# Kernel tuning notes

Measured on AMD Instinct MI355X. Metric: run time of the kernel, lower is better.

Reference implementation:

```python
import jax, jax.numpy as jnp
import numpy as np

HIDDEN = 1024
HEADS = 16
HEAD_DIM = HIDDEN // HEADS


def setup_inputs() -> dict:
    key = jax.random.key(0)
    kx, kq, kk, kv, ko = jax.random.split(key, 5)
    s = 1.0 / np.sqrt(HIDDEN)
    return {
        "x": jax.random.normal(kx, (2, 2048, HIDDEN), dtype=jnp.float32),
        "Wq": jax.random.normal(kq, (HIDDEN, HIDDEN), dtype=jnp.float32) * s,
        "Wk": jax.random.normal(kk, (HIDDEN, HIDDEN), dtype=jnp.float32) * s,
        "Wv": jax.random.normal(kv, (HIDDEN, HIDDEN), dtype=jnp.float32) * s,
        "Wo": jax.random.normal(ko, (HIDDEN, HIDDEN), dtype=jnp.float32) * s,
    }


def reference(x, Wq, Wk, Wv, Wo):
    B, T, C = x.shape
    H, D = HEADS, HEAD_DIM
    # projections (torch Linear: y = x @ W.T); weights here stored as (out,in)==(C,C)
    q = (x @ Wq.T).reshape(B, T, H, D)
    k = (x @ Wk.T).reshape(B, T, H, D)
    v = (x @ Wv.T).reshape(B, T, H, D)
    scale = 1.0 / np.sqrt(D).astype(np.float32)
    # scores: (B,H,T,T)
    attn = jnp.einsum("bqhd,bkhd->bhqk", q, k) * scale
    causal = jnp.tril(jnp.ones((T, T), dtype=bool))  # keep lower triangle
    attn = jnp.where(causal, attn, -jnp.inf)
    attn = jax.nn.softmax(attn, axis=-1)
    out = jnp.einsum("bhqk,bkhd->bqhd", attn, v).reshape(B, T, C)
    return out @ Wo.T
```

## Files before the change

### kernel.cpp

```cpp
#include <hip/hip_runtime.h>
#include <cstdint>
#include <cstddef>

#define HID 1024
#define NH 16
#define HD 64
#define SEQ 2048
#define BATCH 2

typedef __attribute__((ext_vector_type(8))) short bf16x8;
typedef __attribute__((ext_vector_type(4))) short bf16x4;
typedef bf16x8 __attribute__((may_alias)) bf16x8_ma;
typedef bf16x4 __attribute__((may_alias)) bf16x4_ma;
typedef uint4 __attribute__((may_alias)) uint4_ma;
typedef __attribute__((ext_vector_type(4))) float f32x4;

__device__ __forceinline__ unsigned short f2bf(float f){
  unsigned u = __builtin_bit_cast(unsigned, f);
  u += 0x7fffu + ((u >> 16) & 1u);
  return (unsigned short)(u >> 16);
}

__device__ __forceinline__ unsigned cvtpk_bf16(float lo, float hi){
  unsigned r;
  asm("v_cvt_pk_bf16_f32 %0, %1, %2" : "=v"(r) : "v"(lo), "v"(hi));
  return r;
}

__device__ __forceinline__ void gll(const unsigned short* g, unsigned short* l){
  __builtin_amdgcn_global_load_lds(
      (const __attribute__((address_space(1))) unsigned int*)(g),
      (__attribute__((address_space(3))) unsigned int*)(l),
      16, 0, 0);
}


__global__ __launch_bounds__(256) void cvt_all(
    const float* __restrict__ x,  const float* __restrict__ wq,
    const float* __restrict__ wk, const float* __restrict__ wv,
    const float* __restrict__ wo,
    unsigned short* __restrict__ xb,  unsigned short* __restrict__ wqb,
    unsigned short* __restrict__ wkb, unsigned short* __restrict__ wvb,
    unsigned short* __restrict__ wob)
{
  const size_t NX = (size_t)BATCH*SEQ*HID;
  const size_t NW = (size_t)HID*HID;
  size_t i = ((size_t)blockIdx.x*256 + threadIdx.x)*4;
  const float* src; unsigned short* dst; size_t off;
  if (i < NX) { src = x; dst = xb; off = i; }
  else {
    size_t j = i - NX; int w = (int)(j >> 20); off = j & (NW-1);
    if      (w==0){ src=wq; dst=wqb; }
    else if (w==1){ src=wk; dst=wkb; }
    else if (w==2){ src=wv; dst=wvb; }
    else          { src=wo; dst=wob; }
  }
  float4 v = *(const float4*)(src+off);
  uint2 p;
  p.x = (unsigned)f2bf(v.x) | ((unsigned)f2bf(v.y)<<16);
  p.y = (unsigned)f2bf(v.z) | ((unsigned)f2bf(v.w)<<16);
  *(uint2*)(dst+off) = p;
}

__global__ __launch_bounds__(256) void gemm_qkv(
    const unsigned short* __restrict__ A,
    const unsigned short* __restrict__ Bq,
    const unsigned short* __restrict__ Bk,
    const unsigned short* __restrict__ Bv,
    unsigned short* __restrict__ Qh,
    unsigned short* __restrict__ Kh,
    unsigned short* __restrict__ VhT)
{
  __shared__ unsigned short S[16384];
  const int tid = threadIdx.x;
  const int w = tid >> 6, lane = tid & 63, l15 = lane & 15, quad = lane >> 4;
  const int wm = (w >> 1)*64, wn = (w & 1)*64;
  const int bm = blockIdx.y*128;
  const int which = blockIdx.x >> 3;
  const int bn = (blockIdx.x & 7)*128;
  const unsigned short* B = which==0 ? Bq : (which==1 ? Bk : Bv);
  unsigned short* C       = which==0 ? Qh : (which==1 ? Kh : VhT);
  const float cscale      = which==0 ? 0.18033688011112042f : 1.0f;
  const int lrow = lane >> 2;
  const int lcs = (((lane & 3) ^ ((lane >> 3) & 3))) * 8;
  const int qsw = (quad ^ ((l15 >> 1) & 3)) * 8;

  f32x4 acc[4][4] = {};

  {
    #pragma unroll
    for (int p=0;p<2;p++){
      int c = w*2 + p;
      gll(&A[(size_t)(bm + c*16 + lrow)*HID + lcs], &S[c*512]);
      gll(&B[(size_t)(bn + c*16 + lrow)*HID + lcs], &S[8192 + c*512]);
    }
  }
  __syncthreads();

  int cur = 0;
  for (int kb=0; kb<32; ++kb){
    if (kb < 31){
      unsigned short* Ad = S + (cur^1)*4096;
      unsigned short* Bd = S + 8192 + (cur^1)*4096;
      #pragma unroll
      for (int p=0;p<2;p++){
        int c = w*2 + p;
        gll(&A[(size_t)(bm + c*16 + lrow)*HID + (kb+1)*32 + lcs], &Ad[c*512]);
        gll(&B[(size_t)(bn + c*16 + lrow)*HID + (kb+1)*32 + lcs], &Bd[c*512]);
      }
    }
    const unsigned short* Ac = S + cur*4096;
    const unsigned short* Bc = S + 8192 + cur*4096;
    bf16x8 af[4], bfr[4];
    #pragma unroll
    for (int i=0;i<4;i++) af[i]  = *(const bf16x8*)(&Ac[(wm + i*16 + l15)*32 + qsw]);
    #pragma unroll
    for (int j=0;j<4;j++) bfr[j] = *(const bf16x8*)(&Bc[(wn + j*16 + l15)*32 + qsw]);
    #pragma unroll
    for (int i=0;i<4;i++)
      #pragma unroll
      for (int j=0;j<4;j++)
        acc[i][j] = __builtin_amdgcn_mfma_f32_16x16x32_bf16(af[i], bfr[j], acc[i][j], 0,0,0);
    __syncthreads();
    cur ^= 1;
  }

  #pragma unroll
  for (int i=0;i<4;i++)
    #pragma unroll
    for (int j=0;j<4;j++)
      #pragma unroll
      for (int r=0;r<4;r++){
        int row = wm + i*16 + quad*4 + r;
        int col = wn + j*16 + l15;
        unsigned off = (unsigned)(row*256 + col*2);
        *(unsigned short*)((char*)S + (off ^ ((unsigned)(row & 7) << 4))) =
            f2bf(acc[i][j][r]*cscale);
      }
  __syncthreads();
  if (which < 2){
    #pragma unroll
    for (int pass=0; pass<8; ++pass){
      int tr    = pass*16 + (tid >> 4);
      int hf    = (tid >> 3) & 1;
      int blkin = tid & 7;
      unsigned off = (unsigned)(tr*256 + hf*128 + blkin*16);
      uint4 v = *(const uint4_ma*)((const char*)S + (off ^ ((unsigned)(tr & 7) << 4)));
      int m = bm + tr, b = m >> 11, t = m & (SEQ-1);
      int h = (bn >> 6) + hf;
      *(uint4*)(&C[(((size_t)(b*NH + h))*SEQ + t)*HD + blkin*8]) = v;
    }
  } else {
    const int b = bm >> 11, tb = bm & (SEQ-1);
    #pragma unroll
    for (int pass=0; pass<8; ++pass){
      int idx  = pass*256 + tid;
      int dcol = idx & 127;
      int tc   = idx >> 7;
      unsigned short tmp[8];
      #pragma unroll
      for (int j=0;j<8;j++){
        int r = tc*8 + j;
        unsigned off = (unsigned)(r*256 + dcol*2) ^ ((unsigned)j << 4);
        tmp[j] = *(const unsigned short*)((const char*)S + off);
      }
      int hh = (bn >> 6) + (dcol >> 6);
      int d  = dcol & 63;
      *(uint4*)(&C[(((size_t)(b*NH + hh))*HD + d)*SEQ + tb + tc*8]) = *(uint4_ma*)tmp;
    }
  }
}

__global__ __launch_bounds__(256) void gemm_out(
    const unsigned short* __restrict__ A,
    const unsigned short* __restrict__ B,
    float* __restrict__ C)
{
  __shared__ unsigned short S[12288];
  const int tid = threadIdx.x;
  const int w = tid >> 6, lane = tid & 63, l15 = lane & 15, quad = lane >> 4;
  const int wm = (w >> 1)*64, wn = (w & 1)*32;
  const int bm = blockIdx.y*128, bn = blockIdx.x*64;
  const int lrow = lane >> 2;
  const int lcs = (((lane & 3) ^ ((lane >> 3) & 3))) * 8;
  const int qsw = (quad ^ ((l15 >> 1) & 3)) * 8;

  f32x4 acc[4][2] = {};

  {
    #pragma unroll
    for (int p=0;p<2;p++){
      int c = w*2 + p;
      gll(&A[(size_t)(bm + c*16 + lrow)*HID + lcs], &S[c*512]);
    }
    gll(&B[(size_t)(bn + w*16 + lrow)*HID + lcs], &S[8192 + w*512]);
  }
  __syncthreads();

  int cur = 0;
  for (int kb=0; kb<32; ++kb){
    if (kb < 31){
      unsigned short* Ad = S + (cur^1)*4096;
      unsigned short* Bd = S + 8192 + (cur^1)*2048;
      #pragma unroll
      for (int p=0;p<2;p++){
        int c = w*2 + p;
        gll(&A[(size_t)(bm + c*16 + lrow)*HID + (kb+1)*32 + lcs], &Ad[c*512]);
      }
      gll(&B[(size_t)(bn + w*16 + lrow)*HID + (kb+1)*32 + lcs], &Bd[w*512]);
    }
    const unsigned short* Ac = S + cur*4096;
    const unsigned short* Bc = S + 8192 + cur*2048;
    bf16x8 af[4], bfr[2];
    #pragma unroll
    for (int i=0;i<4;i++) af[i]  = *(const bf16x8*)(&Ac[(wm + i*16 + l15)*32 + qsw]);
    #pragma unroll
    for (int j=0;j<2;j++) bfr[j] = *(const bf16x8*)(&Bc[(wn + j*16 + l15)*32 + qsw]);
    #pragma unroll
    for (int i=0;i<4;i++)
      #pragma unroll
      for (int j=0;j<2;j++)
        acc[i][j] = __builtin_amdgcn_mfma_f32_16x16x32_bf16(af[i], bfr[j], acc[i][j], 0,0,0);
    __syncthreads();
    cur ^= 1;
  }

  #pragma unroll
  for (int i=0;i<4;i++)
    #pragma unroll
    for (int j=0;j<2;j++)
      #pragma unroll
      for (int r=0;r<4;r++){
        int m = bm + wm + i*16 + quad*4 + r;
        int n = bn + wn + j*16 + l15;
        C[(size_t)m*HID + n] = acc[i][j][r];
      }
}

__global__ __launch_bounds__(256, 4) void attn(
    const unsigned short* __restrict__ Qh,
    const unsigned short* __restrict__ Kh,
    const unsigned short* __restrict__ VhT,
    unsigned short* __restrict__ Ao)
{
  __shared__ unsigned short QP[4096];
  __shared__ unsigned short Ks[2][4096];
  __shared__ unsigned short Vt[2][4096];

  const int bh = blockIdx.x;
  const int y  = blockIdx.y;
  const int a = y & 7, bb = y >> 3;
  const int qb = (bb & 1) ? (7 - a)*4 + bb : a*4 + bb;
  const int tid = threadIdx.x;
  const int w = tid >> 6, lane = tid & 63, l15 = lane & 15, quad = lane >> 4;
  const int lrow = lane >> 2;
  const int lcs = (((lane & 3) ^ ((lane >> 3) & 3))) * 8;
  const int qsw = (quad ^ ((l15 >> 1) & 3)) * 8;

  const size_t base = (size_t)bh * SEQ * HD;
  const unsigned short* Qg  = Qh + base + (size_t)qb*64*HD;
  const unsigned short* VTg = VhT + base;
  unsigned short* Psw = QP + w*1024;
  const unsigned swz = (unsigned)(l15 & 7) << 4;

  #pragma unroll
  for (int p=0;p<2;p++){
    int c = w*2 + p;
    gll(&Qg[(size_t)((c&3)*16 + lrow)*HD + (c>>2)*32 + lcs], &QP[(c>>2)*2048 + (c&3)*512]);
  }
  {
    const unsigned short* Kg = Kh + base;
    if (w < 2){
      #pragma unroll
      for (int p=0;p<4;p++){ int cc = w*4 + p;
        gll(&Kg[(size_t)((cc&3)*16 + lrow)*HD + (cc>>2)*32 + lcs], &Ks[0][(cc>>2)*2048 + (cc&3)*512]); }
    } else {
      #pragma unroll
      for (int p=0;p<4;p++){ int cc = (w-2)*4 + p;
        gll(&VTg[(size_t)((cc&3)*16 + lrow)*SEQ + (cc>>2)*32 + lcs], &Vt[0][(cc>>2)*2048 + (cc&3)*512]); }
    }
  }
  __syncthreads();
  bf16x8 qfrag[2];
  #pragma unroll
  for (int kc=0;kc<2;kc++)
    qfrag[kc] = *(const bf16x8*)(&QP[kc*2048 + (w*16 + l15)*32 + qsw]);
  __syncthreads();

  f32x4 lacc = {0.f, 0.f, 0.f, 0.f};
  f32x4 oacc[4] = {};
  const int qrow = qb*64 + w*16 + l15;
  int cur = 0;

  for (int kb=0; kb<=qb; ++kb){
    if (kb < qb){
      const unsigned short* Kg2 = Kh + base + (size_t)(kb+1)*64*HD;
      unsigned short* Kd = Ks[cur^1];
      unsigned short* Vd = Vt[cur^1];
      if (w < 2){
        #pragma unroll
        for (int p=0;p<4;p++){ int cc = w*4 + p;
          gll(&Kg2[(size_t)((cc&3)*16 + lrow)*HD + (cc>>2)*32 + lcs], &Kd[(cc>>2)*2048 + (cc&3)*512]); }
      } else {
        #pragma unroll
        for (int p=0;p<4;p++){ int cc = (w-2)*4 + p;
          gll(&VTg[(size_t)((cc&3)*16 + lrow)*SEQ + (size_t)(kb+1)*64 + (cc>>2)*32 + lcs], &Vd[(cc>>2)*2048 + (cc&3)*512]); }
      }
    }

    const unsigned short* Ksc = Ks[cur];
    f32x4 s[4] = {};
    #pragma unroll
    for (int cb=0;cb<4;cb++)
      #pragma unroll
      for (int kc=0;kc<2;kc++){
        bf16x8 kfr = *(const bf16x8*)(&Ksc[kc*2048 + (cb*16 + l15)*32 + qsw]);
        s[cb] = __builtin_amdgcn_mfma_f32_16x16x32_bf16(kfr, qfrag[kc], s[cb], 0,0,0);
      }

    if (kb == qb){
      #pragma unroll
      for (int cb=0;cb<4;cb++)
        #pragma unroll
        for (int r=0;r<4;r++){
          int t = kb*64 + cb*16 + quad*4 + r;
          if (t > qrow) s[cb][r] = -1e30f;
        }
    }
    #pragma unroll
    for (int cb=0;cb<4;cb++)
      #pragma unroll
      for (int r=0;r<4;r++)
        s[cb][r] = exp2f(s[cb][r]);
    lacc += (s[0] + s[1]) + (s[2] + s[3]);

    #pragma unroll
    for (int cb=0;cb<4;cb++){
      uint2 d2;
      d2.x = cvtpk_bf16(s[cb][0], s[cb][1]);
      d2.y = cvtpk_bf16(s[cb][2], s[cb][3]);
      *(bf16x4_ma*)((char*)Psw + (((unsigned)(l15*128 + cb*32 + quad*8)) ^ swz)) =
          __builtin_bit_cast(bf16x4, d2);
    }
    asm volatile("" ::: "memory");
    bf16x8 pa[2];
    #pragma unroll
    for (int kc=0;kc<2;kc++)
      pa[kc] = *(const bf16x8_ma*)((const char*)Psw + (((unsigned)(l15*128 + kc*64 + quad*16)) ^ swz));

    const unsigned short* Vtc = Vt[cur];
    #pragma unroll
    for (int db=0;db<4;db++)
      #pragma unroll
      for (int kc=0;kc<2;kc++){
        bf16x8 vfr = *(const bf16x8*)(&Vtc[kc*2048 + (db*16 + l15)*32 + qsw]);
        oacc[db] = __builtin_amdgcn_mfma_f32_16x16x32_bf16(pa[kc], vfr, oacc[db], 0,0,0);
      }

    if (kb < qb) __syncthreads();
    cur ^= 1;
  }

  float l = (lacc[0] + lacc[1]) + (lacc[2] + lacc[3]);
  l += __shfl_xor(l, 16);
  l += __shfl_xor(l, 32);
  float inv[4];
  #pragma unroll
  for (int r=0;r<4;r++)
    inv[r] = 1.0f / __shfl(l, quad*4 + r);

  const int b = bh >> 4, h = bh & (NH-1);
  #pragma unroll
  for (int db=0;db<4;db++)
    #pragma unroll
    for (int r=0;r<4;r++){
      int t = qb*64 + w*16 + quad*4 + r;
      int col = h*HD + db*16 + l15;
      Ao[((size_t)b*SEQ + t)*HID + col] = f2bf(oacc[db][r] * inv[r]);
    }
}

extern "C" void kernel_launch(void* const* d_in, const int* in_sizes, int n_in,
                              void* d_out, int out_size, void* d_ws, size_t ws_size,
                              hipStream_t stream)
{
  const float* x  = (const float*)d_in[0];
  const float* Wq = (const float*)d_in[1];
  const float* Wk = (const float*)d_in[2];
  const float* Wv = (const float*)d_in[3];
  const float* Wo = (const float*)d_in[4];

  unsigned short* xb  = (unsigned short*)d_ws;
  unsigned short* wqb = xb  + (size_t)4*1024*1024;
  unsigned short* wkb = wqb + (size_t)1024*1024;
  unsigned short* wvb = wkb + (size_t)1024*1024;
  unsigned short* wob = wvb + (size_t)1024*1024;
  unsigned short* Qh  = wob + (size_t)1024*1024;
  unsigned short* Kh  = Qh  + (size_t)4*1024*1024;
  unsigned short* Vh  = Kh  + (size_t)4*1024*1024;
  unsigned short* VhT = Vh  + (size_t)4*1024*1024;
  unsigned short* Ao  = xb;

  cvt_all<<<8192, 256, 0, stream>>>(x, Wq, Wk, Wv, Wo, xb, wqb, wkb, wvb, wob);

  gemm_qkv<<<dim3(24, 32), 256, 0, stream>>>(xb, wqb, wkb, wvb, Qh, Kh, VhT);

  attn<<<dim3(BATCH*NH, SEQ/64), 256, 0, stream>>>(Qh, Kh, VhT, Ao);

  gemm_out<<<dim3(16, 32), 256, 0, stream>>>(Ao, wob, (float*)d_out);
}
```

Measured before the change: 175.2 us.

## Process 128-key tiles per pipeline stage in causal attention kernel

The attention kernel now loads K and V^T in 128-key tiles (two 64-key groups) per double-buffered stage instead of 64, halving the number of loop iterations and __syncthreads barriers. Each stage runs up to two 64-key sub-blocks, skipping the second when it lies past the causal limit. This doubles LDS use for K/V and lowers the launch-bounds occupancy hint from 4 to 2 blocks. Fewer waves can then hide latency, and the last tile may load keys it never uses.

New measurement: 185.2 us. +5.7%, slower.

```diff
diff --git a/kernel.cpp b/kernel.cpp
--- a/kernel.cpp
+++ b/kernel.cpp
@@ -237,15 +237,15 @@
       }
 }
 
-__global__ __launch_bounds__(256, 4) void attn(
+__global__ __launch_bounds__(256, 2) void attn(
     const unsigned short* __restrict__ Qh,
     const unsigned short* __restrict__ Kh,
     const unsigned short* __restrict__ VhT,
     unsigned short* __restrict__ Ao)
 {
   __shared__ unsigned short QP[4096];
-  __shared__ unsigned short Ks[2][4096];
-  __shared__ unsigned short Vt[2][4096];
+  __shared__ unsigned short Ks[2][8192];
+  __shared__ unsigned short Vt[2][8192];
 
   const int bh = blockIdx.x;
   const int y  = blockIdx.y;
@@ -259,6 +259,7 @@
 
   const size_t base = (size_t)bh * SEQ * HD;
   const unsigned short* Qg  = Qh + base + (size_t)qb*64*HD;
+  const unsigned short* Kg  = Kh + base;
   const unsigned short* VTg = VhT + base;
   unsigned short* Psw = QP + w*1024;
   const unsigned swz = (unsigned)(l15 & 7) << 4;
@@ -268,17 +269,14 @@
     int c = w*2 + p;
     gll(&Qg[(size_t)((c&3)*16 + lrow)*HD + (c>>2)*32 + lcs], &QP[(c>>2)*2048 + (c&3)*512]);
   }
-  {
-    const unsigned short* Kg = Kh + base;
-    if (w < 2){
-      #pragma unroll
-      for (int p=0;p<4;p++){ int cc = w*4 + p;
-        gll(&Kg[(size_t)((cc&3)*16 + lrow)*HD + (cc>>2)*32 + lcs], &Ks[0][(cc>>2)*2048 + (cc&3)*512]); }
-    } else {
-      #pragma unroll
-      for (int p=0;p<4;p++){ int cc = (w-2)*4 + p;
-        gll(&VTg[(size_t)((cc&3)*16 + lrow)*SEQ + (cc>>2)*32 + lcs], &Vt[0][(cc>>2)*2048 + (cc&3)*512]); }
-    }
+  if (w < 2){
+    #pragma unroll
+    for (int p=0;p<8;p++){ int cc = w*8 + p; int g = cc>>3, h = (cc>>2)&1, rb = cc&3;
+      gll(&Kg[(size_t)(g*64 + rb*16 + lrow)*HD + h*32 + lcs], &Ks[0][g*4096 + h*2048 + rb*512]); }
+  } else {
+    #pragma unroll
+    for (int p=0;p<8;p++){ int cc = (w-2)*8 + p; int g = cc>>3, h = (cc>>2)&1, rb = cc&3;
+      gll(&VTg[(size_t)(rb*16 + lrow)*SEQ + g*64 + h*32 + lcs], &Vt[0][g*4096 + h*2048 + rb*512]); }
   }
   __syncthreads();
   bf16x8 qfrag[2];
@@ -290,74 +288,82 @@
   f32x4 lacc = {0.f, 0.f, 0.f, 0.f};
   f32x4 oacc[4] = {};
   const int qrow = qb*64 + w*16 + l15;
+  const int qmax = qb*64 + 63;
+  const int nt = (qb >> 1) + 1;
   int cur = 0;
 
-  for (int kb=0; kb<=qb; ++kb){
-    if (kb < qb){
-      const unsigned short* Kg2 = Kh + base + (size_t)(kb+1)*64*HD;
-      unsigned short* Kd = Ks[cur^1];
-      unsigned short* Vd = Vt[cur^1];
+  for (int kb=0; kb<nt; ++kb){
+    if (kb+1 < nt){
       if (w < 2){
         #pragma unroll
-        for (int p=0;p<4;p++){ int cc = w*4 + p;
-          gll(&Kg2[(size_t)((cc&3)*16 + lrow)*HD + (cc>>2)*32 + lcs], &Kd[(cc>>2)*2048 + (cc&3)*512]); }
+        for (int p=0;p<8;p++){ int cc = w*8 + p; int g = cc>>3, h = (cc>>2)&1, rb = cc&3;
+          gll(&Kg[(size_t)((kb+1)*128 + g*64 + rb*16 + lrow)*HD + h*32 + lcs],
+              &Ks[cur^1][g*4096 + h*2048 + rb*512]); }
       } else {
         #pragma unroll
-        for (int p=0;p<4;p++){ int cc = (w-2)*4 + p;
-          gll(&VTg[(size_t)((cc&3)*16 + lrow)*SEQ + (size_t)(kb+1)*64 + (cc>>2)*32 + lcs], &Vd[(cc>>2)*2048 + (cc&3)*512]); }
-      }
-    }
-
+        for (int p=0;p<8;p++){ int cc = (w-2)*8 + p; int g = cc>>3, h = (cc>>2)&1, rb = cc&3;
+          gll(&VTg[(size_t)(rb*16 + lrow)*SEQ + (size_t)(kb+1)*128 + g*64 + h*32 + lcs],
+              &Vt[cur^1][g*4096 + h*2048 + rb*512]); }
+      }
+    }
     const unsigned short* Ksc = Ks[cur];
-    f32x4 s[4] = {};
-    #pragma unroll
-    for (int cb=0;cb<4;cb++)
-      #pragma unroll
-      for (int kc=0;kc<2;kc++){
-        bf16x8 kfr = *(const bf16x8*)(&Ksc[kc*2048 + (cb*16 + l15)*32 + qsw]);
-        s[cb] = __builtin_amdgcn_mfma_f32_16x16x32_bf16(kfr, qfrag[kc], s[cb], 0,0,0);
-      }
-
-    if (kb == qb){
-      #pragma unroll
-      for (int cb=0;cb<4;cb++)
-        #pragma unroll
-        for (int r=0;r<4;r++){
-          int t = kb*64 + cb*16 + quad*4 + r;
-          if (t > qrow) s[cb][r] = -1e30f;
+    const unsigned short* Vtc = Vt[cur];
+    const bool lastt = (kb == nt-1);
+
+    #pragma unroll
+    for (int g=0; g<2; ++g){
+      const int kstart = kb*128 + g*64;
+      if (kstart <= qmax){
+        f32x4 s[4] = {};
+        #pragma unroll
+        for (int cb=0;cb<4;cb++)
+          #pragma unroll
+          for (int kc=0;kc<2;kc++){
+            bf16x8 kfr = *(const bf16x8*)(&Ksc[g*4096 + kc*2048 + (cb*16 + l15)*32 + qsw]);
+            s[cb] = __builtin_amdgcn_mfma_f32_16x16x32_bf16(kfr, qfrag[kc], s[cb], 0,0,0);
+          }
+        if (lastt){
+          #pragma unroll
+          for (int cb=0;cb<4;cb++)
+            #pragma unroll
+            for (int r=0;r<4;r++){
+              int t = kstart + cb*16 + quad*4 + r;
+              if (t > qrow) s[cb][r] = -1e30f;
+            }
         }
-    }
-    #pragma unroll
-    for (int cb=0;cb<4;cb++)
-      #pragma unroll
-      for (int r=0;r<4;r++)
-        s[cb][r] = exp2f(s[cb][r]);
-    lacc += (s[0] + s[1]) + (s[2] + s[3]);
-
-    #pragma unroll
-    for (int cb=0;cb<4;cb++){
-      uint2 d2;
-      d2.x = cvtpk_bf16(s[cb][0], s[cb][1]);
-      d2.y = cvtpk_bf16(s[cb][2], s[cb][3]);
-      *(bf16x4_ma*)((char*)Psw + (((unsigned)(l15*128 + cb*32 + quad*8)) ^ swz)) =
-          __builtin_bit_cast(bf16x4, d2);
-    }
-    asm volatile("" ::: "memory");
-    bf16x8 pa[2];
-    #pragma unroll
-    for (int kc=0;kc<2;kc++)
-      pa[kc] = *(const bf16x8_ma*)((const char*)Psw + (((unsigned)(l15*128 + kc*64 + quad*16)) ^ swz));
-
-    const unsigned short* Vtc = Vt[cur];
-    #pragma unroll
-    for (int db=0;db<4;db++)
-      #pragma unroll
-      for (int kc=0;kc<2;kc++){
-        bf16x8 vfr = *(const bf16x8*)(&Vtc[kc*2048 + (db*16 + l15)*32 + qsw]);
-        oacc[db] = __builtin_amdgcn_mfma_f32_16x16x32_bf16(pa[kc], vfr, oacc[db], 0,0,0);
-      }
-
-    if (kb < qb) __syncthreads();
+        #pragma unroll
+        for (int cb=0;cb<4;cb++)
+          #pragma unroll
+          for (int r=0;r<4;r++)
+            s[cb][r] = exp2f(s[cb][r]);
+        lacc += (s[0] + s[1]) + (s[2] + s[3]);
+
+        #pragma unroll
+        for (int cb=0;cb<4;cb++){
+          uint2 d2;
+          d2.x = cvtpk_bf16(s[cb][0], s[cb][1]);
+          d2.y = cvtpk_bf16(s[cb][2], s[cb][3]);
+          *(bf16x4_ma*)((char*)Psw + (((unsigned)(l15*128 + cb*32 + quad*8)) ^ swz)) =
+              __builtin_bit_cast(bf16x4, d2);
+        }
+        asm volatile("" ::: "memory");
+        bf16x8 pa[2];
+        #pragma unroll
+        for (int kc=0;kc<2;kc++)
+          pa[kc] = *(const bf16x8_ma*)((const char*)Psw + (((unsigned)(l15*128 + kc*64 + quad*16)) ^ swz));
+
+        #pragma unroll
+        for (int db=0;db<4;db++)
+          #pragma unroll
+          for (int kc=0;kc<2;kc++){
+            bf16x8 vfr = *(const bf16x8*)(&Vtc[g*4096 + kc*2048 + (db*16 + l15)*32 + qsw]);
+            oacc[db] = __builtin_amdgcn_mfma_f32_16x16x32_bf16(pa[kc], vfr, oacc[db], 0,0,0);
+          }
+        asm volatile("" ::: "memory");
+      }
+    }
+
+    if (kb+1 < nt) __syncthreads();
     cur ^= 1;
   }
 
```

## Widen attention query tile to 128 rows with eight waves sharing K/V tiles

Applied to the files above, without the earlier changes.

The attention kernel now gives each block 128 query rows handled by 8 wavefronts (512 threads) instead of 64 rows with 4 waves. Each K/V tile loaded into LDS is therefore reused by twice as many query rows, roughly halving K/V global and LDS fill traffic per query. The cost is half as many blocks and higher register and occupancy pressure under the new launch bounds. On the diagonal block, the lower waves also compute a fully masked extra key tile. The causal load-balancing pairing of query blocks is remapped for 16 query blocks.

After: 178.7 us. About the same (+2.0%).

```diff
diff --git a/kernel.cpp b/kernel.cpp
--- a/kernel.cpp
+++ b/kernel.cpp
@@ -237,20 +237,19 @@
       }
 }
 
-__global__ __launch_bounds__(256, 4) void attn(
+__global__ __launch_bounds__(512, 4) void attn(
     const unsigned short* __restrict__ Qh,
     const unsigned short* __restrict__ Kh,
     const unsigned short* __restrict__ VhT,
     unsigned short* __restrict__ Ao)
 {
-  __shared__ unsigned short QP[4096];
+  __shared__ unsigned short QP[8192];
   __shared__ unsigned short Ks[2][4096];
   __shared__ unsigned short Vt[2][4096];
 
   const int bh = blockIdx.x;
   const int y  = blockIdx.y;
-  const int a = y & 7, bb = y >> 3;
-  const int qb = (bb & 1) ? (7 - a)*4 + bb : a*4 + bb;
+  const int qb = (y < 8) ? y : 23 - y;
   const int tid = threadIdx.x;
   const int w = tid >> 6, lane = tid & 63, l15 = lane & 15, quad = lane >> 4;
   const int lrow = lane >> 2;
@@ -258,7 +257,8 @@
   const int qsw = (quad ^ ((l15 >> 1) & 3)) * 8;
 
   const size_t base = (size_t)bh * SEQ * HD;
-  const unsigned short* Qg  = Qh + base + (size_t)qb*64*HD;
+  const unsigned short* Qg  = Qh + base + (size_t)qb*128*HD;
+  const unsigned short* Kg  = Kh + base;
   const unsigned short* VTg = VhT + base;
   unsigned short* Psw = QP + w*1024;
   const unsigned swz = (unsigned)(l15 & 7) << 4;
@@ -266,45 +266,40 @@
   #pragma unroll
   for (int p=0;p<2;p++){
     int c = w*2 + p;
-    gll(&Qg[(size_t)((c&3)*16 + lrow)*HD + (c>>2)*32 + lcs], &QP[(c>>2)*2048 + (c&3)*512]);
-  }
-  {
-    const unsigned short* Kg = Kh + base;
-    if (w < 2){
-      #pragma unroll
-      for (int p=0;p<4;p++){ int cc = w*4 + p;
-        gll(&Kg[(size_t)((cc&3)*16 + lrow)*HD + (cc>>2)*32 + lcs], &Ks[0][(cc>>2)*2048 + (cc&3)*512]); }
-    } else {
-      #pragma unroll
-      for (int p=0;p<4;p++){ int cc = (w-2)*4 + p;
-        gll(&VTg[(size_t)((cc&3)*16 + lrow)*SEQ + (cc>>2)*32 + lcs], &Vt[0][(cc>>2)*2048 + (cc&3)*512]); }
-    }
+    gll(&Qg[(size_t)((c&7)*16 + lrow)*HD + (c>>3)*32 + lcs], &QP[(c>>3)*4096 + (c&7)*512]);
+  }
+  if (w < 4){
+    #pragma unroll
+    for (int p=0;p<2;p++){ int cc = (w&3)*2 + p; int h = cc>>2, rb = cc&3;
+      gll(&Kg[(size_t)(rb*16 + lrow)*HD + h*32 + lcs], &Ks[0][h*2048 + rb*512]); }
+  } else {
+    #pragma unroll
+    for (int p=0;p<2;p++){ int cc = (w-4)*2 + p; int h = cc>>2, rb = cc&3;
+      gll(&VTg[(size_t)(rb*16 + lrow)*SEQ + h*32 + lcs], &Vt[0][h*2048 + rb*512]); }
   }
   __syncthreads();
   bf16x8 qfrag[2];
   #pragma unroll
   for (int kc=0;kc<2;kc++)
-    qfrag[kc] = *(const bf16x8*)(&QP[kc*2048 + (w*16 + l15)*32 + qsw]);
+    qfrag[kc] = *(const bf16x8*)(&QP[kc*4096 + (w*16 + l15)*32 + qsw]);
   __syncthreads();
 
   f32x4 lacc = {0.f, 0.f, 0.f, 0.f};
   f32x4 oacc[4] = {};
-  const int qrow = qb*64 + w*16 + l15;
+  const int qrow = qb*128 + w*16 + l15;
+  const int nt = 2*qb + 2;
   int cur = 0;
 
-  for (int kb=0; kb<=qb; ++kb){
-    if (kb < qb){
-      const unsigned short* Kg2 = Kh + base + (size_t)(kb+1)*64*HD;
-      unsigned short* Kd = Ks[cur^1];
-      unsigned short* Vd = Vt[cur^1];
-      if (w < 2){
+  for (int kb=0; kb<nt; ++kb){
+    if (kb+1 < nt){
+      if (w < 4){
         #pragma unroll
-        for (int p=0;p<4;p++){ int cc = w*4 + p;
-          gll(&Kg2[(size_t)((cc&3)*16 + lrow)*HD + (cc>>2)*32 + lcs], &Kd[(cc>>2)*2048 + (cc&3)*512]); }
+        for (int p=0;p<2;p++){ int cc = (w&3)*2 + p; int h = cc>>2, rb = cc&3;
+          gll(&Kg[(size_t)((kb+1)*64 + rb*16 + lrow)*HD + h*32 + lcs], &Ks[cur^1][h*2048 + rb*512]); }
       } else {
         #pragma unroll
-        for (int p=0;p<4;p++){ int cc = (w-2)*4 + p;
-          gll(&VTg[(size_t)((cc&3)*16 + lrow)*SEQ + (size_t)(kb+1)*64 + (cc>>2)*32 + lcs], &Vd[(cc>>2)*2048 + (cc&3)*512]); }
+        for (int p=0;p<2;p++){ int cc = (w-4)*2 + p; int h = cc>>2, rb = cc&3;
+          gll(&VTg[(size_t)(rb*16 + lrow)*SEQ + (size_t)(kb+1)*64 + h*32 + lcs], &Vt[cur^1][h*2048 + rb*512]); }
       }
     }
 
@@ -318,7 +313,7 @@
         s[cb] = __builtin_amdgcn_mfma_f32_16x16x32_bf16(kfr, qfrag[kc], s[cb], 0,0,0);
       }
 
-    if (kb == qb){
+    if (kb >= 2*qb){
       #pragma unroll
       for (int cb=0;cb<4;cb++)
         #pragma unroll
@@ -357,7 +352,7 @@
         oacc[db] = __builtin_amdgcn_mfma_f32_16x16x32_bf16(pa[kc], vfr, oacc[db], 0,0,0);
       }
 
-    if (kb < qb) __syncthreads();
+    if (kb+1 < nt) __syncthreads();
     cur ^= 1;
   }
 
@@ -374,7 +369,7 @@
   for (int db=0;db<4;db++)
     #pragma unroll
     for (int r=0;r<4;r++){
-      int t = qb*64 + w*16 + quad*4 + r;
+      int t = qb*128 + w*16 + quad*4 + r;
       int col = h*HD + db*16 + l15;
       Ao[((size_t)b*SEQ + t)*HID + col] = f2bf(oacc[db][r] * inv[r]);
     }
@@ -405,7 +400,7 @@
 
   gemm_qkv<<<dim3(24, 32), 256, 0, stream>>>(xb, wqb, wkb, wvb, Qh, Kh, VhT);
 
-  attn<<<dim3(BATCH*NH, SEQ/64), 256, 0, stream>>>(Qh, Kh, VhT, Ao);
+  attn<<<dim3(BATCH*NH, 16), 512, 0, stream>>>(Qh, Kh, VhT, Ao);
 
   gemm_out<<<dim3(16, 32), 256, 0, stream>>>(Ao, wob, (float*)d_out);
 }
```

## Split attention KV loop across two wave groups with LDS merge

Applied to the files above, without the earlier changes.

The attention block grows to 512 threads, arranged as two groups of four waves. Each group processes alternating 32-key halves of every 64-key tile, and the partial outputs and row sums are merged through shared memory at the end. The double-buffered K/V prefetch is replaced by a single buffer that is loaded after a barrier, so each step now takes two syncs and loads are no longer overlapped with compute. The aim is more waves in flight and shorter per-wave serial chains. In exchange it adds merge overhead, extra barriers, and the loss of the load/compute overlap.

Measured after the change: 189.1 us. +7.9%, slower.

```diff
diff --git a/kernel.cpp b/kernel.cpp
--- a/kernel.cpp
+++ b/kernel.cpp
@@ -237,15 +237,15 @@
       }
 }
 
-__global__ __launch_bounds__(256, 4) void attn(
+__global__ __launch_bounds__(512, 8) void attn(
     const unsigned short* __restrict__ Qh,
     const unsigned short* __restrict__ Kh,
     const unsigned short* __restrict__ VhT,
     unsigned short* __restrict__ Ao)
 {
-  __shared__ unsigned short QP[4096];
-  __shared__ unsigned short Ks[2][4096];
-  __shared__ unsigned short Vt[2][4096];
+  __shared__ unsigned short QP[8192];
+  __shared__ unsigned short Ks[4096];
+  __shared__ unsigned short Vt[4096];
 
   const int bh = blockIdx.x;
   const int y  = blockIdx.y;
@@ -253,131 +253,144 @@
   const int qb = (bb & 1) ? (7 - a)*4 + bb : a*4 + bb;
   const int tid = threadIdx.x;
   const int w = tid >> 6, lane = tid & 63, l15 = lane & 15, quad = lane >> 4;
+  const int g = w >> 2, wq = w & 3;
   const int lrow = lane >> 2;
   const int lcs = (((lane & 3) ^ ((lane >> 3) & 3))) * 8;
   const int qsw = (quad ^ ((l15 >> 1) & 3)) * 8;
 
   const size_t base = (size_t)bh * SEQ * HD;
   const unsigned short* Qg  = Qh + base + (size_t)qb*64*HD;
+  const unsigned short* Kg  = Kh + base;
   const unsigned short* VTg = VhT + base;
-  unsigned short* Psw = QP + w*1024;
-  const unsigned swz = (unsigned)(l15 & 7) << 4;
-
+  char* Psw = (char*)QP + w*2048;
+
+  {
+    int rb = w & 3, kc = w >> 2;
+    gll(&Qg[(size_t)(rb*16 + lrow)*HD + kc*32 + lcs], &QP[kc*2048 + rb*512]);
+  }
   #pragma unroll
   for (int p=0;p<2;p++){
     int c = w*2 + p;
-    gll(&Qg[(size_t)((c&3)*16 + lrow)*HD + (c>>2)*32 + lcs], &QP[(c>>2)*2048 + (c&3)*512]);
-  }
-  {
-    const unsigned short* Kg = Kh + base;
-    if (w < 2){
-      #pragma unroll
-      for (int p=0;p<4;p++){ int cc = w*4 + p;
-        gll(&Kg[(size_t)((cc&3)*16 + lrow)*HD + (cc>>2)*32 + lcs], &Ks[0][(cc>>2)*2048 + (cc&3)*512]); }
+    if (c < 8){
+      int tt = c >> 2, cc = c & 3, kc = cc >> 1, cb = cc & 1;
+      gll(&Kg[(size_t)(tt*32 + cb*16 + lrow)*HD + kc*32 + lcs],
+          &Ks[tt*2048 + kc*1024 + cb*512]);
     } else {
-      #pragma unroll
-      for (int p=0;p<4;p++){ int cc = (w-2)*4 + p;
-        gll(&VTg[(size_t)((cc&3)*16 + lrow)*SEQ + (cc>>2)*32 + lcs], &Vt[0][(cc>>2)*2048 + (cc&3)*512]); }
+      int tt = (c >> 2) & 1, cc = c & 3;
+      gll(&VTg[(size_t)(cc*16 + lrow)*SEQ + tt*32 + lcs],
+          &Vt[tt*2048 + cc*512]);
     }
   }
   __syncthreads();
   bf16x8 qfrag[2];
   #pragma unroll
   for (int kc=0;kc<2;kc++)
-    qfrag[kc] = *(const bf16x8*)(&QP[kc*2048 + (w*16 + l15)*32 + qsw]);
+    qfrag[kc] = *(const bf16x8*)(&QP[kc*2048 + (wq*16 + l15)*32 + qsw]);
   __syncthreads();
 
   f32x4 lacc = {0.f, 0.f, 0.f, 0.f};
   f32x4 oacc[4] = {};
-  const int qrow = qb*64 + w*16 + l15;
-  int cur = 0;
-
-  for (int kb=0; kb<=qb; ++kb){
-    if (kb < qb){
-      const unsigned short* Kg2 = Kh + base + (size_t)(kb+1)*64*HD;
-      unsigned short* Kd = Ks[cur^1];
-      unsigned short* Vd = Vt[cur^1];
-      if (w < 2){
-        #pragma unroll
-        for (int p=0;p<4;p++){ int cc = w*4 + p;
-          gll(&Kg2[(size_t)((cc&3)*16 + lrow)*HD + (cc>>2)*32 + lcs], &Kd[(cc>>2)*2048 + (cc&3)*512]); }
-      } else {
-        #pragma unroll
-        for (int p=0;p<4;p++){ int cc = (w-2)*4 + p;
-          gll(&VTg[(size_t)((cc&3)*16 + lrow)*SEQ + (size_t)(kb+1)*64 + (cc>>2)*32 + lcs], &Vd[(cc>>2)*2048 + (cc&3)*512]); }
-      }
-    }
-
-    const unsigned short* Ksc = Ks[cur];
-    f32x4 s[4] = {};
-    #pragma unroll
-    for (int cb=0;cb<4;cb++)
+  const int qrow = qb*64 + wq*16 + l15;
+
+  for (int si=0; si<=qb; ++si){
+    const int kt = 2*si + g;
+
+    f32x4 s[2] = {};
+    #pragma unroll
+    for (int cb=0;cb<2;cb++)
       #pragma unroll
       for (int kc=0;kc<2;kc++){
-        bf16x8 kfr = *(const bf16x8*)(&Ksc[kc*2048 + (cb*16 + l15)*32 + qsw]);
+        bf16x8 kfr = *(const bf16x8*)(&Ks[g*2048 + kc*1024 + (cb*16 + l15)*32 + qsw]);
         s[cb] = __builtin_amdgcn_mfma_f32_16x16x32_bf16(kfr, qfrag[kc], s[cb], 0,0,0);
       }
-
-    if (kb == qb){
-      #pragma unroll
-      for (int cb=0;cb<4;cb++)
+    if (si == qb){
+      #pragma unroll
+      for (int cb=0;cb<2;cb++)
         #pragma unroll
         for (int r=0;r<4;r++){
-          int t = kb*64 + cb*16 + quad*4 + r;
+          int t = kt*32 + cb*16 + quad*4 + r;
           if (t > qrow) s[cb][r] = -1e30f;
         }
     }
     #pragma unroll
-    for (int cb=0;cb<4;cb++)
+    for (int cb=0;cb<2;cb++)
       #pragma unroll
       for (int r=0;r<4;r++)
         s[cb][r] = exp2f(s[cb][r]);
-    lacc += (s[0] + s[1]) + (s[2] + s[3]);
-
-    #pragma unroll
-    for (int cb=0;cb<4;cb++){
+    lacc += s[0] + s[1];
+
+    #pragma unroll
+    for (int cb=0;cb<2;cb++){
       uint2 d2;
       d2.x = cvtpk_bf16(s[cb][0], s[cb][1]);
       d2.y = cvtpk_bf16(s[cb][2], s[cb][3]);
-      *(bf16x4_ma*)((char*)Psw + (((unsigned)(l15*128 + cb*32 + quad*8)) ^ swz)) =
-          __builtin_bit_cast(bf16x4, d2);
+      *(bf16x4_ma*)(Psw + l15*80 + cb*32 + quad*8) = __builtin_bit_cast(bf16x4, d2);
     }
     asm volatile("" ::: "memory");
-    bf16x8 pa[2];
-    #pragma unroll
-    for (int kc=0;kc<2;kc++)
-      pa[kc] = *(const bf16x8_ma*)((const char*)Psw + (((unsigned)(l15*128 + kc*64 + quad*16)) ^ swz));
-
-    const unsigned short* Vtc = Vt[cur];
-    #pragma unroll
-    for (int db=0;db<4;db++)
-      #pragma unroll
-      for (int kc=0;kc<2;kc++){
-        bf16x8 vfr = *(const bf16x8*)(&Vtc[kc*2048 + (db*16 + l15)*32 + qsw]);
-        oacc[db] = __builtin_amdgcn_mfma_f32_16x16x32_bf16(pa[kc], vfr, oacc[db], 0,0,0);
-      }
-
-    if (kb < qb) __syncthreads();
-    cur ^= 1;
+    bf16x8 pa = *(const bf16x8_ma*)(Psw + l15*80 + quad*16);
+
+    #pragma unroll
+    for (int db=0;db<4;db++){
+      bf16x8 vfr = *(const bf16x8*)(&Vt[g*2048 + (db*16 + l15)*32 + qsw]);
+      oacc[db] = __builtin_amdgcn_mfma_f32_16x16x32_bf16(pa, vfr, oacc[db], 0,0,0);
+    }
+
+    __syncthreads();
+    if (si < qb){
+      #pragma unroll
+      for (int p=0;p<2;p++){
+        int c = w*2 + p;
+        if (c < 8){
+          int tt = c >> 2, cc = c & 3, kc = cc >> 1, cb = cc & 1;
+          gll(&Kg[(size_t)((2*si+2+tt)*32 + cb*16 + lrow)*HD + kc*32 + lcs],
+              &Ks[tt*2048 + kc*1024 + cb*512]);
+        } else {
+          int tt = (c >> 2) & 1, cc = c & 3;
+          gll(&VTg[(size_t)(cc*16 + lrow)*SEQ + (size_t)(2*si+2+tt)*32 + lcs],
+              &Vt[tt*2048 + cc*512]);
+        }
+      }
+      __syncthreads();
+    }
   }
 
   float l = (lacc[0] + lacc[1]) + (lacc[2] + lacc[3]);
   l += __shfl_xor(l, 16);
   l += __shfl_xor(l, 32);
-  float inv[4];
-  #pragma unroll
-  for (int r=0;r<4;r++)
-    inv[r] = 1.0f / __shfl(l, quad*4 + r);
-
-  const int b = bh >> 4, h = bh & (NH-1);
-  #pragma unroll
-  for (int db=0;db<4;db++)
-    #pragma unroll
-    for (int r=0;r<4;r++){
-      int t = qb*64 + w*16 + quad*4 + r;
-      int col = h*HD + db*16 + l15;
-      Ao[((size_t)b*SEQ + t)*HID + col] = f2bf(oacc[db][r] * inv[r]);
-    }
+
+  float* MRG = (float*)QP;
+  float* Lb  = (float*)Ks;
+  if (g == 1){
+    #pragma unroll
+    for (int db=0;db<4;db++)
+      #pragma unroll
+      for (int r=0;r<4;r++)
+        MRG[wq*1024 + (quad*4 + r)*64 + db*16 + l15] = oacc[db][r];
+    Lb[wq*16 + l15] = l;
+  }
+  __syncthreads();
+  if (g == 0){
+    l += Lb[wq*16 + l15];
+    #pragma unroll
+    for (int db=0;db<4;db++)
+      #pragma unroll
+      for (int r=0;r<4;r++)
+        oacc[db][r] += MRG[wq*1024 + (quad*4 + r)*64 + db*16 + l15];
+    float inv[4];
+    #pragma unroll
+    for (int r=0;r<4;r++)
+      inv[r] = 1.0f / __shfl(l, quad*4 + r);
+
+    const int b = bh >> 4, h = bh & (NH-1);
+    #pragma unroll
+    for (int db=0;db<4;db++)
+      #pragma unroll
+      for (int r=0;r<4;r++){
+        int t = qb*64 + wq*16 + quad*4 + r;
+        int col = h*HD + db*16 + l15;
+        Ao[((size_t)b*SEQ + t)*HID + col] = f2bf(oacc[db][r] * inv[r]);
+      }
+  }
 }
 
 extern "C" void kernel_launch(void* const* d_in, const int* in_sizes, int n_in,
@@ -405,7 +418,7 @@
 
   gemm_qkv<<<dim3(24, 32), 256, 0, stream>>>(xb, wqb, wkb, wvb, Qh, Kh, VhT);
 
-  attn<<<dim3(BATCH*NH, SEQ/64), 256, 0, stream>>>(Qh, Kh, VhT, Ao);
+  attn<<<dim3(BATCH*NH, SEQ/64), 512, 0, stream>>>(Qh, Kh, VhT, Ao);
 
   gemm_out<<<dim3(16, 32), 256, 0, stream>>>(Ao, wob, (float*)d_out);
 }
```
